# Optimization experiments

Measured on AMD Instinct MI355X. Metric: run time of the kernel, lower is better.

The kernel has to match this reference:

```python
import jax, jax.numpy as jnp
import numpy as np

NUM_HEADS = 12
C_HEAD_DIM = 4   # int(1/dim_ratio)
S_HEAD_DIM = 16  # head_dim * dim_ratio
HEAD_DIM = C_HEAD_DIM * S_HEAD_DIM  # 64


def setup_inputs() -> dict:
    key = jax.random.key(0)
    ks = jax.random.split(key, 5)
    B, N, C, D = 8, 196, 12, 768
    x = jax.random.normal(ks[0], (B, N, C, D), dtype=jnp.float32)
    w_qkv_c = jax.random.normal(ks[1], (NUM_HEADS * 3 * C_HEAD_DIM, D), dtype=jnp.float32) * 0.02
    w_qkv_s = jax.random.normal(ks[2], (NUM_HEADS * 3 * S_HEAD_DIM, D), dtype=jnp.float32) * 0.02
    w_proj = jax.random.normal(ks[3], (D, D), dtype=jnp.float32) * 0.02
    b_proj = jnp.zeros((D,), dtype=jnp.float32)
    return {"x": x, "w_qkv_c": w_qkv_c, "w_qkv_s": w_qkv_s, "w_proj": w_proj, "b_proj": b_proj}


def _sdpa(q, k, v):
    # PyTorch F.scaled_dot_product_attention default scale: 1/sqrt(q.shape[-1])
    scale = q.shape[-1] ** -0.5
    attn = jax.nn.softmax(jnp.einsum('...qd,...kd->...qk', q * scale, k), axis=-1)
    return jnp.einsum('...qk,...kd->...qd', attn, v)


def reference(x, w_qkv_c, w_qkv_s, w_proj, b_proj):
    B, N, C, D = x.shape
    H, chd, shd = NUM_HEADS, C_HEAD_DIM, S_HEAD_DIM
    # channel-attention qkv: (3, B, H, N, C, chd)
    qkv_c = (x @ w_qkv_c.T).reshape(B, N, C, 3, H, chd).transpose(3, 0, 4, 1, 2, 5)
    qc, kc, vc = qkv_c[0], qkv_c[1], qkv_c[2]
    # spatial-attention qkv: (3, B, H, N, C, shd) -> attend over N
    qkv_s = (x @ w_qkv_s.T).reshape(B, N, C, 3, H, shd).transpose(3, 0, 4, 1, 2, 5)
    qs, ks, vs = qkv_s[0], qkv_s[1], qkv_s[2]
    qs, ks, vs = (t.swapaxes(-2, -3) for t in (qs, ks, vs))  # (B,H,C,N,shd)
    # spatial attention over N, then back to (B,H,N,C,shd)
    xs = _sdpa(qs, ks, vs).swapaxes(-2, -3)
    # channel attention over C: (B,H,N,C,chd)
    xc = _sdpa(qc, kc, vc)
    # outer product combine: (B,H,N,C,chd,shd) -> (B,H,N,C,head_dim)
    out = (xc[..., :, None] * xs[..., None, :]).reshape(B, H, N, C, chd * shd)
    # (B,N,H,C,hd) -> reshape (B,N,C,D) (row-major, matches torch)
    out = out.swapaxes(1, 2).reshape(B, N, C, D)
    return out @ w_proj.T + b_proj
```

## Files before the change

kernel.cpp:

```cpp
#include <hip/hip_runtime.h>
#include <math.h>

#define B_  8
#define N_  196
#define C_  12
#define D_  768
#define H_  12
#define R_  (B_*N_*C_)
#define KDIM 768
#define NQKV_PAD 768

typedef _Float16 f16x8 __attribute__((ext_vector_type(8)));
typedef _Float16 f16x4 __attribute__((ext_vector_type(4)));
typedef __fp16 fp16x2 __attribute__((ext_vector_type(2)));
typedef __attribute__((ext_vector_type(4))) float f32x4;

__device__ inline unsigned short f2h(float f) {
    union { _Float16 h; unsigned short u; } v; v.h = (_Float16)f; return v.u;
}
__device__ inline float h2f(unsigned short u) {
    union { unsigned short u; _Float16 h; } v; v.u = u; return (float)v.h;
}
__device__ inline unsigned pk2u(float a, float b) {
    union { fp16x2 h; unsigned u; } v;
    v.h = __builtin_amdgcn_cvt_pkrtz(a, b);
    return v.u;
}

__global__ __launch_bounds__(256) void convert_all(
    const float* __restrict__ x,
    const float* __restrict__ wc, const float* __restrict__ ws,
    const float* __restrict__ wp,
    unsigned short* __restrict__ xh,
    unsigned short* __restrict__ wqkv_h, unsigned short* __restrict__ wp_h)
{
    int i = (blockIdx.x * 256 + threadIdx.x) * 4;
    const int NX = R_ * KDIM;
    float4 v; unsigned short* dh; int off;
    if (i < NX) {
        v = *reinterpret_cast<const float4*>(x + i);
        dh = xh; off = i;
    } else if (i < NX + 768 * 768) {
        off = i - NX;
        const int r = off / 768, k = off % 768;
        v = make_float4(0.f, 0.f, 0.f, 0.f);
        if (r < 144)      v = *reinterpret_cast<const float4*>(wc + r * 768 + k);
        else if (r < 720) v = *reinterpret_cast<const float4*>(ws + (r - 144) * 768 + k);
        dh = wqkv_h;
    } else {
        off = i - NX - 768 * 768;
        if (off >= 768 * 768) return;
        v = *reinterpret_cast<const float4*>(wp + off);
        dh = wp_h;
    }
    uint2 h;
    h.x = pk2u(v.x, v.y);
    h.y = pk2u(v.z, v.w);
    *reinterpret_cast<uint2*>(dh + off) = h;
}

#define BM 128
#define BN 128
#define BK 64

__device__ inline void gload16(const unsigned short* src, void* ldsbase) {
    __builtin_amdgcn_global_load_lds(
        (const __attribute__((address_space(1))) unsigned int*)src,
        (__attribute__((address_space(3))) unsigned int*)ldsbase, 16, 0, 0);
}

__global__ __launch_bounds__(512, 2) void gemm_f16(
    const unsigned short* __restrict__ Ah, const unsigned short* __restrict__ Bh,
    const float* __restrict__ bias,
    float* __restrict__ outp, unsigned short* __restrict__ outh,
    int M, int Nt, int K, int ntiles)
{
    __shared__ unsigned short sA[2][BM][BK];
    __shared__ unsigned short sB[2][BN][BK];

    const int nwg = gridDim.x;
    const int bid = blockIdx.x;
    const int xcd = bid & 7, slot = bid >> 3;
    const int q = nwg >> 3, r = nwg & 7;
    const int wg = (xcd < r ? xcd * (q + 1) : r * (q + 1) + (xcd - r) * q) + slot;
    const int mt = wg / ntiles, nt = wg - mt * ntiles;
    const int m0 = mt * BM, n0 = nt * BN;

    const int tid = threadIdx.x;
    const int w = tid >> 6, l = tid & 63;
    const int fl = l & 15, g = l >> 4;
    const int wr = (w >> 2) * 64;
    const int wc = (w & 3) * 32;

    f32x4 acc[4][2];
    #pragma unroll
    for (int i = 0; i < 4; ++i)
        #pragma unroll
        for (int j = 0; j < 2; ++j)
            acc[i][j] = (f32x4){0.f, 0.f, 0.f, 0.f};

    const int srow = w * 16 + (l >> 3);
    const int scol = ((l & 7) ^ (l >> 3)) * 8;

#define STAGE(buf, kk) {                                                                    \
    const unsigned short* pa = Ah + (size_t)(m0 + srow) * K + (kk) + scol;                  \
    const unsigned short* pb = Bh + (size_t)(n0 + srow) * K + (kk) + scol;                  \
    char* da = (char*)sA + (buf) * 16384 + w * 2048;                                        \
    char* db = (char*)sB + (buf) * 16384 + w * 2048;                                        \
    gload16(pa,          da);                                                               \
    gload16(pa + 8 * K,  da + 1024);                                                        \
    gload16(pb,          db);                                                               \
    gload16(pb + 8 * K,  db + 1024); }

    STAGE(0, 0);

    const int KT = K / BK;
    int cur = 0;
    for (int t = 0; t < KT; ++t) {
        if (t + 1 < KT) {
            STAGE(cur ^ 1, (t + 1) * BK);
            asm volatile("s_waitcnt vmcnt(4)" ::: "memory");
        } else {
            asm volatile("s_waitcnt vmcnt(0)" ::: "memory");
        }
        asm volatile("s_barrier" ::: "memory");

        #pragma unroll
        for (int ks = 0; ks < 2; ++ks) {
            const int rcol = ((ks * 4 + g) ^ (fl & 7)) * 8;
            f16x8 ah[4];
            #pragma unroll
            for (int fm = 0; fm < 4; ++fm)
                ah[fm] = *reinterpret_cast<const f16x8*>(&sA[cur][wr + fm * 16 + fl][rcol]);
            #pragma unroll
            for (int fn = 0; fn < 2; ++fn) {
                const f16x8 bf = *reinterpret_cast<const f16x8*>(&sB[cur][wc + fn * 16 + fl][rcol]);
                #pragma unroll
                for (int fm = 0; fm < 4; ++fm)
                    acc[fm][fn] = __builtin_amdgcn_mfma_f32_16x16x32_f16(ah[fm], bf, acc[fm][fn], 0, 0, 0);
            }
        }
        asm volatile("s_barrier" ::: "memory");
        cur ^= 1;
    }
#undef STAGE

    const int rg = g * 4;
    if (outh) {
        #pragma unroll
        for (int fm = 0; fm < 4; ++fm)
            #pragma unroll
            for (int fn = 0; fn < 2; ++fn) {
                const int row = m0 + wr + fm * 16 + rg;
                const int col = n0 + wc + fn * 16 + fl;
                #pragma unroll
                for (int rr = 0; rr < 4; ++rr)
                    outh[(size_t)(row + rr) * Nt + col] = f2h(acc[fm][fn][rr]);
            }
    } else {
        #pragma unroll
        for (int fm = 0; fm < 4; ++fm)
            #pragma unroll
            for (int fn = 0; fn < 2; ++fn) {
                const int row = m0 + wr + fm * 16 + rg;
                const int col = n0 + wc + fn * 16 + fl;
                const float bv = bias ? bias[col] : 0.f;
                #pragma unroll
                for (int rr = 0; rr < 4; ++rr)
                    outp[(size_t)(row + rr) * Nt + col] = acc[fm][fn][rr] + bv;
            }
    }
}

__global__ __launch_bounds__(256) void spatial_attn_mfma(
    const unsigned short* __restrict__ qkv,
    unsigned short* __restrict__ xs_out)
{
    __shared__ unsigned short Kl[224][24];
    __shared__ unsigned short Ql[208][24];
    __shared__ unsigned short Vt[16][236];

    const int bid2 = blockIdx.x;
    const int half = bid2 & 1;
    const int bid = bid2 >> 1;
    const int c = bid % 12;
    const int h = (bid / 12) % 12;
    const int b = bid / 144;
    const int tid = threadIdx.x;
    const int w = tid >> 6, l = tid & 63;
    const int fl = l & 15, g = l >> 4;
    const int qbase = half * 7;
    const int ntl = 7 - half;

    const float qs = 0.25f * 1.4426950408889634f;
    for (int idx = tid; idx < N_ * 4; idx += 256) {
        const int n = idx >> 2, eq = (idx & 3) * 4;
        const unsigned short* base =
            qkv + (size_t)((b * N_ + n) * 12 + c) * NQKV_PAD + 144 + h * 16 + eq;
        const ushort4 qv = *reinterpret_cast<const ushort4*>(base);
        const ushort4 kv = *reinterpret_cast<const ushort4*>(base + 192);
        const ushort4 vv = *reinterpret_cast<const ushort4*>(base + 384);
        uint2 qsc;
        qsc.x = pk2u(h2f(qv.x) * qs, h2f(qv.y) * qs);
        qsc.y = pk2u(h2f(qv.z) * qs, h2f(qv.w) * qs);
        *reinterpret_cast<uint2*>(&Ql[n][eq]) = qsc;
        *reinterpret_cast<ushort4*>(&Kl[n][eq]) = kv;
        Vt[eq + 0][n] = vv.x;
        Vt[eq + 1][n] = vv.y;
        Vt[eq + 2][n] = vv.z;
        Vt[eq + 3][n] = vv.w;
    }
    for (int idx = tid; idx < 16 * 28; idx += 256) {
        const int d = idx / 28, n = 196 + idx % 28;
        Vt[d][n] = 0;
    }
    __syncthreads();

    f32x4 accO[2];
    float lsum[2];
    #pragma unroll
    for (int j = 0; j < 2; ++j) {
        accO[j] = (f32x4){0.f, 0.f, 0.f, 0.f};
        lsum[j] = 0.f;
    }
    const f32x4 zf = (f32x4){0.f, 0.f, 0.f, 0.f};

    f16x4 Bq[2];
    #pragma unroll
    for (int j = 0; j < 2; ++j) {
        const int qtl = w + 4 * j;
        const int qt = (qtl < ntl) ? (qbase + qtl) : 12;
        Bq[j] = *reinterpret_cast<const f16x4*>(&Ql[qt * 16 + fl][4 * g]);
    }

    for (int ch = 0; ch < 7; ++ch) {
        const int kb0 = ch * 32;
        const f16x4 Ak0 = *reinterpret_cast<const f16x4*>(&Kl[kb0 + fl][4 * g]);
        const f16x4 Ak1 = *reinterpret_cast<const f16x4*>(&Kl[kb0 + 16 + fl][4 * g]);
        const f16x4 Av0 = *reinterpret_cast<const f16x4*>(&Vt[fl][kb0 + 4 * g]);
        const f16x4 Av1 = *reinterpret_cast<const f16x4*>(&Vt[fl][kb0 + 16 + 4 * g]);

        #pragma unroll
        for (int j = 0; j < 2; ++j) {
            if (w + 4 * j >= ntl) continue;

            f32x4 T0 = __builtin_amdgcn_mfma_f32_16x16x16f16(Ak0, Bq[j], zf, 0, 0, 0);
            f32x4 T1 = __builtin_amdgcn_mfma_f32_16x16x16f16(Ak1, Bq[j], zf, 0, 0, 0);

            float s0 = T0[0], s1 = T0[1], s2 = T0[2], s3 = T0[3];
            float s4 = T1[0], s5 = T1[1], s6 = T1[2], s7 = T1[3];
            if (ch == 6) {
                const int kg = kb0 + 4 * g;
                if (kg + 0 >= 196) s0 = -1e30f;
                if (kg + 1 >= 196) s1 = -1e30f;
                if (kg + 2 >= 196) s2 = -1e30f;
                if (kg + 3 >= 196) s3 = -1e30f;
                s4 = -1e30f; s5 = -1e30f; s6 = -1e30f; s7 = -1e30f;
            }
            const float p0 = exp2f(s0), p1 = exp2f(s1);
            const float p2 = exp2f(s2), p3 = exp2f(s3);
            const float p4 = exp2f(s4), p5 = exp2f(s5);
            const float p6 = exp2f(s6), p7 = exp2f(s7);
            lsum[j] += ((p0 + p1) + (p2 + p3)) + ((p4 + p5) + (p6 + p7));

            union { unsigned u[2]; f16x4 v; } pa, pb;
            pa.u[0] = pk2u(p0, p1); pa.u[1] = pk2u(p2, p3);
            pb.u[0] = pk2u(p4, p5); pb.u[1] = pk2u(p6, p7);

            accO[j] = __builtin_amdgcn_mfma_f32_16x16x16f16(Av0, pa.v, accO[j], 0, 0, 0);
            accO[j] = __builtin_amdgcn_mfma_f32_16x16x16f16(Av1, pb.v, accO[j], 0, 0, 0);
        }
    }

    #pragma unroll
    for (int j = 0; j < 2; ++j) {
        const int qtl = w + 4 * j;
        if (qtl >= ntl) continue;
        const int qt = qbase + qtl;
        float ls = lsum[j];
        ls += __shfl_xor(ls, 16);
        ls += __shfl_xor(ls, 32);
        const int n = qt * 16 + fl;
        if (n < 196) {
            const float inv = 1.f / ls;
            uint2 o;
            o.x = pk2u(accO[j][0] * inv, accO[j][1] * inv);
            o.y = pk2u(accO[j][2] * inv, accO[j][3] * inv);
            const size_t base = ((size_t)((b * 12 + h) * N_ + n) * 12 + c) * 16 + 4 * g;
            *reinterpret_cast<uint2*>(&xs_out[base]) = o;
        }
    }
}

__global__ __launch_bounds__(256) void chan_attn_combine4(
    const unsigned short* __restrict__ qkv,
    const unsigned short* __restrict__ xs,
    unsigned short* __restrict__ yh)
{
    const int sub = threadIdx.x >> 6;
    const int t = threadIdx.x & 63;
    const int flat = blockIdx.x * 4 + sub;
    const int n = flat % 196;
    const int h = (flat / 196) % 12;
    const int b = flat / 2352;

    __shared__ float sQ[4][12][4], sK[4][12][4], sV[4][12][4], sXc[4][12][4];
    __shared__ float sXs[4][12][16];

    for (int idx = t; idx < 144; idx += 64) {
        const int c = idx / 12, rem = idx % 12, s = rem >> 2, e = rem & 3;
        const float v = h2f(qkv[(size_t)((b * N_ + n) * 12 + c) * NQKV_PAD + s * 48 + h * 4 + e]);
        if (s == 0) sQ[sub][c][e] = v;
        else if (s == 1) sK[sub][c][e] = v;
        else sV[sub][c][e] = v;
    }
    for (int idx = t; idx < 192; idx += 64) {
        const int c = idx >> 4, j = idx & 15;
        sXs[sub][c][j] = h2f(xs[((size_t)flat * 12 + c) * 16 + j]);
    }
    __syncthreads();

    if (t < 12) {
        const int c = t;
        float s[12];
        float m = -INFINITY;
        #pragma unroll
        for (int c2 = 0; c2 < 12; ++c2) {
            float d = 0.f;
            #pragma unroll
            for (int e = 0; e < 4; ++e) d += sQ[sub][c][e] * sK[sub][c2][e];
            s[c2] = d * 0.5f;
            m = fmaxf(m, s[c2]);
        }
        float lsum = 0.f;
        #pragma unroll
        for (int c2 = 0; c2 < 12; ++c2) { s[c2] = __expf(s[c2] - m); lsum += s[c2]; }
        const float inv = 1.f / lsum;
        #pragma unroll
        for (int i = 0; i < 4; ++i) {
            float a = 0.f;
            #pragma unroll
            for (int c2 = 0; c2 < 12; ++c2) a += s[c2] * sV[sub][c2][i];
            sXc[sub][c][i] = a * inv;
        }
    }
    __syncthreads();

    const size_t yrow = ((size_t)(b * N_ + n) * 12 + h) * (size_t)D_;
    #pragma unroll
    for (int k = 0; k < 12; ++k) {
        const float v = sXc[sub][k][t >> 4] * sXs[sub][k][t & 15];
        yh[yrow + k * 64 + t] = f2h(v);
    }
}

extern "C" void kernel_launch(void* const* d_in, const int* in_sizes, int n_in,
                              void* d_out, int out_size, void* d_ws, size_t ws_size,
                              hipStream_t stream) {
    const float* x       = (const float*)d_in[0];
    const float* w_qkv_c = (const float*)d_in[1];
    const float* w_qkv_s = (const float*)d_in[2];
    const float* w_proj  = (const float*)d_in[3];
    const float* b_proj  = (const float*)d_in[4];
    float* out = (float*)d_out;

    unsigned short* xh     = (unsigned short*)d_ws;
    unsigned short* wqkv_h = xh + (size_t)R_ * KDIM;
    unsigned short* wp_h   = wqkv_h + (size_t)768 * 768;
    unsigned short* qkv_h  = wp_h + (size_t)768 * 768;
    unsigned short* xs_h   = qkv_h + (size_t)R_ * NQKV_PAD;
    unsigned short* yh = xh;

    {
        const int total = (R_ * KDIM + 2 * 768 * 768) / 4;
        convert_all<<<(total + 255) / 256, 256, 0, stream>>>(
            x, w_qkv_c, w_qkv_s, w_proj, xh, wqkv_h, wp_h);
    }
    {
        const int mtiles = R_ / BM, ntiles = NQKV_PAD / BN;
        gemm_f16<<<mtiles * ntiles, 512, 0, stream>>>(
            xh, wqkv_h, nullptr, nullptr, qkv_h, R_, NQKV_PAD, KDIM, ntiles);
    }
    spatial_attn_mfma<<<B_ * H_ * C_ * 2, 256, 0, stream>>>(qkv_h, xs_h);
    chan_attn_combine4<<<(B_ * H_ * N_) / 4, 256, 0, stream>>>(qkv_h, xs_h, yh);
    {
        const int mtiles = R_ / BM, ntiles = D_ / BN;
        gemm_f16<<<mtiles * ntiles, 512, 0, stream>>>(
            yh, wp_h, b_proj, out, nullptr, R_, D_, KDIM, ntiles);
    }
}
```

Baseline: 130.4 us.

## Fuse fp32-to-fp16 input conversion into QKV GEMM A-tile loading

Removes the separate pass that converted the activation tensor x to fp16. The QKV GEMM now loads fp32 A tiles through registers, packs them to fp16 and writes them into LDS, prefetching two stages ahead, while B still uses direct global-to-LDS loads. This is meant to eliminate a full read/write pass over the large input, at the cost of reading fp32 A in the GEMM and spending more register pressure and latency on the A path. The weight conversion kernel is kept but now only handles weights.

```diff
diff --git a/kernel.cpp b/kernel.cpp
--- a/kernel.cpp
+++ b/kernel.cpp
@@ -27,28 +27,22 @@
     return v.u;
 }
 
-__global__ __launch_bounds__(256) void convert_all(
-    const float* __restrict__ x,
+__global__ __launch_bounds__(256) void convert_weights(
     const float* __restrict__ wc, const float* __restrict__ ws,
     const float* __restrict__ wp,
-    unsigned short* __restrict__ xh,
     unsigned short* __restrict__ wqkv_h, unsigned short* __restrict__ wp_h)
 {
     int i = (blockIdx.x * 256 + threadIdx.x) * 4;
-    const int NX = R_ * KDIM;
     float4 v; unsigned short* dh; int off;
-    if (i < NX) {
-        v = *reinterpret_cast<const float4*>(x + i);
-        dh = xh; off = i;
-    } else if (i < NX + 768 * 768) {
-        off = i - NX;
+    if (i < 768 * 768) {
+        off = i;
         const int r = off / 768, k = off % 768;
         v = make_float4(0.f, 0.f, 0.f, 0.f);
         if (r < 144)      v = *reinterpret_cast<const float4*>(wc + r * 768 + k);
         else if (r < 720) v = *reinterpret_cast<const float4*>(ws + (r - 144) * 768 + k);
         dh = wqkv_h;
     } else {
-        off = i - NX - 768 * 768;
+        off = i - 768 * 768;
         if (off >= 768 * 768) return;
         v = *reinterpret_cast<const float4*>(wp + off);
         dh = wp_h;
@@ -69,11 +63,119 @@
         (__attribute__((address_space(3))) unsigned int*)ldsbase, 16, 0, 0);
 }
 
+__global__ __launch_bounds__(512, 2) void gemm_qkv_fused(
+    const float* __restrict__ Af, const unsigned short* __restrict__ Bh,
+    unsigned short* __restrict__ outh, int M, int Nt, int K, int ntiles)
+{
+    __shared__ unsigned short sA[2][BM][BK];
+    __shared__ unsigned short sB[2][BN][BK];
+
+    const int nwg = gridDim.x;
+    const int bid = blockIdx.x;
+    const int xcd = bid & 7, slot = bid >> 3;
+    const int q = nwg >> 3, r = nwg & 7;
+    const int wg = (xcd < r ? xcd * (q + 1) : r * (q + 1) + (xcd - r) * q) + slot;
+    const int mt = wg / ntiles, nt = wg - mt * ntiles;
+    const int m0 = mt * BM, n0 = nt * BN;
+
+    const int tid = threadIdx.x;
+    const int w = tid >> 6, l = tid & 63;
+    const int fl = l & 15, g = l >> 4;
+    const int wr = (w >> 2) * 64;
+    const int wc = (w & 3) * 32;
+
+    f32x4 acc[4][2];
+    #pragma unroll
+    for (int i = 0; i < 4; ++i)
+        #pragma unroll
+        for (int j = 0; j < 2; ++j)
+            acc[i][j] = (f32x4){0.f, 0.f, 0.f, 0.f};
+
+    const int srow = w * 16 + (l >> 3);
+    const int scol = ((l & 7) ^ (l >> 3)) * 8;
+
+    float4 a0, a1, a2, a3;
+
+#define LOADA(kk) {                                                                         \
+    const float* paf = Af + (size_t)(m0 + srow) * K + (kk) + scol;                          \
+    a0 = *reinterpret_cast<const float4*>(paf);                                             \
+    a1 = *reinterpret_cast<const float4*>(paf + 4);                                         \
+    a2 = *reinterpret_cast<const float4*>(paf + 8 * K);                                     \
+    a3 = *reinterpret_cast<const float4*>(paf + 8 * K + 4); }
+
+#define WRITEA(buf) {                                                                       \
+    char* da = (char*)sA + (buf) * 16384 + w * 2048 + l * 16;                               \
+    uint4 v0 = { pk2u(a0.x,a0.y), pk2u(a0.z,a0.w), pk2u(a1.x,a1.y), pk2u(a1.z,a1.w) };      \
+    uint4 v1 = { pk2u(a2.x,a2.y), pk2u(a2.z,a2.w), pk2u(a3.x,a3.y), pk2u(a3.z,a3.w) };      \
+    *reinterpret_cast<uint4*>(da) = v0;                                                     \
+    *reinterpret_cast<uint4*>(da + 1024) = v1; }
+
+#define STAGEB(buf, kk) {                                                                   \
+    const unsigned short* pb = Bh + (size_t)(n0 + srow) * K + (kk) + scol;                  \
+    char* db = (char*)sB + (buf) * 16384 + w * 2048;                                        \
+    gload16(pb,          db);                                                               \
+    gload16(pb + 8 * K,  db + 1024); }
+
+    LOADA(0);
+    STAGEB(0, 0);
+    asm volatile("s_waitcnt vmcnt(2)" ::: "memory");
+    WRITEA(0);
+    LOADA(BK);
+    asm volatile("s_waitcnt lgkmcnt(0)" ::: "memory");
+
+    const int KT = K / BK;
+    int cur = 0;
+    for (int t = 0; t < KT; ++t) {
+        if (t + 1 < KT) {
+            STAGEB(cur ^ 1, (t + 1) * BK);
+            asm volatile("s_waitcnt vmcnt(2)" ::: "memory");
+            WRITEA(cur ^ 1);
+            if (t + 2 < KT) LOADA((t + 2) * BK);
+            asm volatile("s_waitcnt lgkmcnt(0)" ::: "memory");
+        } else {
+            asm volatile("s_waitcnt vmcnt(0) lgkmcnt(0)" ::: "memory");
+        }
+        asm volatile("s_barrier" ::: "memory");
+
+        #pragma unroll
+        for (int ks = 0; ks < 2; ++ks) {
+            const int rcol = ((ks * 4 + g) ^ (fl & 7)) * 8;
+            f16x8 ah[4];
+            #pragma unroll
+            for (int fm = 0; fm < 4; ++fm)
+                ah[fm] = *reinterpret_cast<const f16x8*>(&sA[cur][wr + fm * 16 + fl][rcol]);
+            #pragma unroll
+            for (int fn = 0; fn < 2; ++fn) {
+                const f16x8 bf = *reinterpret_cast<const f16x8*>(&sB[cur][wc + fn * 16 + fl][rcol]);
+                #pragma unroll
+                for (int fm = 0; fm < 4; ++fm)
+                    acc[fm][fn] = __builtin_amdgcn_mfma_f32_16x16x32_f16(ah[fm], bf, acc[fm][fn], 0, 0, 0);
+            }
+        }
+        asm volatile("s_barrier" ::: "memory");
+        cur ^= 1;
+    }
+#undef LOADA
+#undef WRITEA
+#undef STAGEB
+
+    const int rg = g * 4;
+    #pragma unroll
+    for (int fm = 0; fm < 4; ++fm)
+        #pragma unroll
+        for (int fn = 0; fn < 2; ++fn) {
+            const int row = m0 + wr + fm * 16 + rg;
+            const int col = n0 + wc + fn * 16 + fl;
+            #pragma unroll
+            for (int rr = 0; rr < 4; ++rr)
+                outh[(size_t)(row + rr) * Nt + col] = f2h(acc[fm][fn][rr]);
+        }
+}
+
 __global__ __launch_bounds__(512, 2) void gemm_f16(
     const unsigned short* __restrict__ Ah, const unsigned short* __restrict__ Bh,
     const float* __restrict__ bias,
-    float* __restrict__ outp, unsigned short* __restrict__ outh,
-    int M, int Nt, int K, int ntiles)
+    float* __restrict__ outp, int M, int Nt, int K, int ntiles)
 {
     __shared__ unsigned short sA[2][BM][BK];
     __shared__ unsigned short sB[2][BN][BK];
@@ -146,30 +248,17 @@
 #undef STAGE
 
     const int rg = g * 4;
-    if (outh) {
-        #pragma unroll
-        for (int fm = 0; fm < 4; ++fm)
-            #pragma unroll
-            for (int fn = 0; fn < 2; ++fn) {
-                const int row = m0 + wr + fm * 16 + rg;
-                const int col = n0 + wc + fn * 16 + fl;
-                #pragma unroll
-                for (int rr = 0; rr < 4; ++rr)
-                    outh[(size_t)(row + rr) * Nt + col] = f2h(acc[fm][fn][rr]);
-            }
-    } else {
-        #pragma unroll
-        for (int fm = 0; fm < 4; ++fm)
-            #pragma unroll
-            for (int fn = 0; fn < 2; ++fn) {
-                const int row = m0 + wr + fm * 16 + rg;
-                const int col = n0 + wc + fn * 16 + fl;
-                const float bv = bias ? bias[col] : 0.f;
-                #pragma unroll
-                for (int rr = 0; rr < 4; ++rr)
-                    outp[(size_t)(row + rr) * Nt + col] = acc[fm][fn][rr] + bv;
-            }
-    }
+    #pragma unroll
+    for (int fm = 0; fm < 4; ++fm)
+        #pragma unroll
+        for (int fn = 0; fn < 2; ++fn) {
+            const int row = m0 + wr + fm * 16 + rg;
+            const int col = n0 + wc + fn * 16 + fl;
+            const float bv = bias[col];
+            #pragma unroll
+            for (int rr = 0; rr < 4; ++rr)
+                outp[(size_t)(row + rr) * Nt + col] = acc[fm][fn][rr] + bv;
+        }
 }
 
 __global__ __launch_bounds__(256) void spatial_attn_mfma(
@@ -364,28 +453,27 @@
     const float* b_proj  = (const float*)d_in[4];
     float* out = (float*)d_out;
 
-    unsigned short* xh     = (unsigned short*)d_ws;
-    unsigned short* wqkv_h = xh + (size_t)R_ * KDIM;
+    unsigned short* yh     = (unsigned short*)d_ws;
+    unsigned short* wqkv_h = yh + (size_t)R_ * KDIM;
     unsigned short* wp_h   = wqkv_h + (size_t)768 * 768;
     unsigned short* qkv_h  = wp_h + (size_t)768 * 768;
     unsigned short* xs_h   = qkv_h + (size_t)R_ * NQKV_PAD;
-    unsigned short* yh = xh;
 
     {
-        const int total = (R_ * KDIM + 2 * 768 * 768) / 4;
-        convert_all<<<(total + 255) / 256, 256, 0, stream>>>(
-            x, w_qkv_c, w_qkv_s, w_proj, xh, wqkv_h, wp_h);
+        const int total = (2 * 768 * 768) / 4;
+        convert_weights<<<(total + 255) / 256, 256, 0, stream>>>(
+            w_qkv_c, w_qkv_s, w_proj, wqkv_h, wp_h);
     }
     {
         const int mtiles = R_ / BM, ntiles = NQKV_PAD / BN;
-        gemm_f16<<<mtiles * ntiles, 512, 0, stream>>>(
-            xh, wqkv_h, nullptr, nullptr, qkv_h, R_, NQKV_PAD, KDIM, ntiles);
+        gemm_qkv_fused<<<mtiles * ntiles, 512, 0, stream>>>(
+            x, wqkv_h, qkv_h, R_, NQKV_PAD, KDIM, ntiles);
     }
     spatial_attn_mfma<<<B_ * H_ * C_ * 2, 256, 0, stream>>>(qkv_h, xs_h);
     chan_attn_combine4<<<(B_ * H_ * N_) / 4, 256, 0, stream>>>(qkv_h, xs_h, yh);
     {
         const int mtiles = R_ / BM, ntiles = D_ / BN;
         gemm_f16<<<mtiles * ntiles, 512, 0, stream>>>(
-            yh, wp_h, b_proj, out, nullptr, R_, D_, KDIM, ntiles);
-    }
-}
+            yh, wp_h, b_proj, out, R_, D_, KDIM, ntiles);
+    }
+}
```

Result: faster. 126.8 us (-2.8%).
